# Optimization experiments

Hardware: AMD Instinct MI355X
Metric: run time of the kernel (lower is better)

## Reference

```python
import jax, jax.numpy as jnp
import numpy as np

B, C, N, H, K = 4, 128, 2048, 4, 20
_BN = np.float32(np.sqrt(1.0 + 1e-5))  # eval BatchNorm: running_mean=0, running_var=1


def setup_inputs() -> dict:
    key = jax.random.key(0)
    ks = jax.random.split(key, 16)
    r = lambda k, s: jax.random.normal(k, s, jnp.float32) * 0.1
    u = lambda k, s: jax.random.uniform(k, s, jnp.float32, 0.5, 1.5)
    return {
        "x": jax.random.normal(ks[0], (B, C, N, 1), jnp.float32),
        "fW": r(ks[1], (3, C, C)),
        "fb": r(ks[2], (3, C)),
        "fg": u(ks[3], (3, C)),
        "fbe": r(ks[4], (3, C)),
        "gW1": r(ks[5], (3, C, 2 * C)),
        "gb1": r(ks[6], (3, C)),
        "gg1": u(ks[7], (3, C)),
        "gbe1": r(ks[8], (3, C)),
        "gW2": r(ks[9], (3, C, C)),
        "gb2": r(ks[10], (3, C)),
        "gg2": u(ks[11], (3, C)),
        "gbe2": r(ks[12], (3, C)),
        "pW": r(ks[13], (C, C)),
        "pb": r(ks[14], (C,)),
        "temp": jnp.ones((H, 1, 1), jnp.float32),
        "num_heads": H,
        "k_num": K,
    }


def _filter(x, W, b, g, be):
    # x: [B,C,N]; 1x1 conv -> InstanceNorm(eps=1e-3) -> eval BatchNorm -> ReLU
    y = jnp.einsum('oc,bcn->bon', W, x) + b[:, None]
    m = jnp.mean(y, -1, keepdims=True)
    v = jnp.var(y, -1, keepdims=True)
    y = (y - m) / jnp.sqrt(v + 1e-3)
    return jax.nn.relu(y / _BN * g[:, None] + be[:, None])


def _knn(x, k):
    # x: [B,C,N]; topk of negative squared distance (self included)
    xx = jnp.sum(x * x, axis=1)                     # [B,N]
    inner = jnp.einsum('bcn,bcm->bnm', x, x)        # [B,N,N]
    pd = 2.0 * inner - xx[:, :, None] - xx[:, None, :]
    return jax.lax.top_k(pd, k)[1]                  # [B,N,k]


def _gcn(x, k, W1, b1, g1, be1, W2, b2, g2, be2):
    idx = _knn(x, k)
    xT = jnp.transpose(x, (0, 2, 1))                # [B,N,C]
    nb = jax.vmap(lambda p, i: p[i])(xT, idx)       # [B,N,k,C]
    ctr = jnp.broadcast_to(xT[:, :, None, :], nb.shape)
    feat = jnp.concatenate([ctr, ctr - nb], axis=-1)  # [B,N,k,2C]
    h = jnp.einsum('oi,bnki->bnko', W1, feat) + b1
    h = jax.nn.relu(h / _BN * g1 + be1)
    h = jnp.einsum('oi,bnki->bnko', W2, h) + b2
    h = jax.nn.relu(h / _BN * g2 + be2)
    return jnp.transpose(jnp.max(h, axis=2), (0, 2, 1))  # [B,C,N]


def _l2norm(x):
    n = jnp.sqrt(jnp.sum(x * x, axis=-1, keepdims=True))
    return x / jnp.maximum(n, 1e-12)


def reference(x, fW, fb, fg, fbe, gW1, gb1, gg1, gbe1, gW2, gb2, gg2, gbe2, pW, pb, temp, num_heads, k_num):
    xin = x[..., 0]                                 # [B,C,N]
    Bn, Cc, Nn = xin.shape
    qkv = []
    for i in range(3):  # q, k, v branches (structurally distinct params)
        f = _filter(xin, fW[i], fb[i], fg[i], fbe[i])
        g = _gcn(f, k_num, gW1[i], gb1[i], gg1[i], gbe1[i], gW2[i], gb2[i], gg2[i], gbe2[i])
        qkv.append(g.reshape(Bn, num_heads, Cc // num_heads, Nn))
    q, kk, v = qkv
    q = _l2norm(q)
    kk = _l2norm(kk)
    attn = jnp.einsum('bhcn,bhdn->bhcd', q, kk) * temp  # channel attention [B,H,c,c]
    attn = jax.nn.softmax(attn, axis=-1)
    out = jnp.einsum('bhcd,bhdn->bhcn', attn, v).reshape(Bn, Cc, Nn)
    out = jnp.einsum('oc,bcn->bon', pW, out) + pb[:, None]
    return (out + xin)[..., None]                   # [B,C,N,1]
```

## Files before the change

kernel.cpp:

```cpp
#include <hip/hip_runtime.h>
#include <math.h>


#define B_ 4
#define C_ 128
#define N_ 2048
#define H_ 4
#define K_ 20

typedef __bf16 bf16x8 __attribute__((ext_vector_type(8)));
typedef float f32x4 __attribute__((ext_vector_type(4)));
typedef unsigned int u32x4 __attribute__((ext_vector_type(4)));

__device__ __forceinline__ unsigned short f2bf(float f) {
    unsigned int u = __builtin_bit_cast(unsigned int, f);
    u += 0x7fffu + ((u >> 16) & 1u);
    return (unsigned short)(u >> 16);
}
__device__ __forceinline__ float bf2f(unsigned short s) {
    return __builtin_bit_cast(float, (unsigned int)s << 16);
}

#define PD_STRIDE 4194304
#define OFF_Y     0
#define OFF_P     0
#define OFF_Q     3145728
#define OFF_GT    6291456
#define OFF_AV    9437184
#define OFF_FT    16777216
#define OFF_SC    19922944
#define OFF_SH    19924480
#define OFF_XX    19926016
#define OFF_IDX   19950592
#define OFF_G     20442112
#define OFF_NRM   23587840
#define OFF_ATT   23588864

__global__ __launch_bounds__(256) void k_filter_conv(
    const float* __restrict__ x, const float* __restrict__ fW,
    const float* __restrict__ fb, float* __restrict__ y)
{
    __shared__ float Ws[8][C_];
    const int n = blockIdx.x * 256 + threadIdx.x;
    const int o0 = blockIdx.y * 8;
    const int iz = blockIdx.z;
    const int i = iz >> 2, b = iz & 3;
    for (int t = threadIdx.x; t < 8 * C_; t += 256) {
        const int j = t >> 7, c = t & 127;
        Ws[j][c] = fW[((size_t)i * C_ + o0 + j) * C_ + c];
    }
    __syncthreads();
    float acc[8] = {};
    const float* xb = x + ((size_t)b * C_) * N_ + n;
    #pragma unroll 4
    for (int c = 0; c < C_; ++c) {
        const float xv = xb[(size_t)c * N_];
        #pragma unroll
        for (int j = 0; j < 8; ++j) acc[j] += Ws[j][c] * xv;
    }
    float* yb = y + ((size_t)iz * C_ + o0) * N_ + n;
    #pragma unroll
    for (int j = 0; j < 8; ++j) yb[(size_t)j * N_] = acc[j] + fb[i * C_ + o0 + j];
}

__global__ __launch_bounds__(256) void k_rowstats(
    const float* __restrict__ y, const float* __restrict__ fg,
    const float* __restrict__ fbe, float* __restrict__ scale, float* __restrict__ shift)
{
    const int r = blockIdx.x;
    const int i = r >> 9, o = r & 127;
    const float* row = y + (size_t)r * N_;
    float s = 0.f, ss = 0.f;
    for (int n = threadIdx.x; n < N_; n += 256) {
        const float v = row[n];
        s += v; ss += v * v;
    }
    #pragma unroll
    for (int off = 32; off > 0; off >>= 1) {
        s += __shfl_down(s, off);
        ss += __shfl_down(ss, off);
    }
    __shared__ float red[2][4];
    const int wid = threadIdx.x >> 6;
    if ((threadIdx.x & 63) == 0) { red[0][wid] = s; red[1][wid] = ss; }
    __syncthreads();
    if (threadIdx.x == 0) {
        s = red[0][0] + red[0][1] + red[0][2] + red[0][3];
        ss = red[1][0] + red[1][1] + red[1][2] + red[1][3];
        const float mean = s * (1.f / N_);
        const float var = ss * (1.f / N_) - mean * mean;
        const float bn = sqrtf(1.00001f);
        const float sc = fg[i * C_ + o] / (bn * sqrtf(var + 1e-3f));
        scale[r] = sc;
        shift[r] = fbe[i * C_ + o] - mean * sc;
    }
}

__global__ __launch_bounds__(256) void k_norm_transpose(
    const float* __restrict__ y, const float* __restrict__ scale,
    const float* __restrict__ shift, float* __restrict__ fT,
    unsigned short* __restrict__ fH, unsigned short* __restrict__ fL)
{
    __shared__ float tile[32][33];
    const int n0 = blockIdx.x * 32, o0 = blockIdx.y * 32;
    const int iz = blockIdx.z;
    const int tx = threadIdx.x, ty = threadIdx.y;
    #pragma unroll
    for (int q = 0; q < 4; ++q) {
        const int o = o0 + ty + q * 8;
        const int r = iz * C_ + o;
        const float v = y[(size_t)r * N_ + n0 + tx] * scale[r] + shift[r];
        tile[ty + q * 8][tx] = fmaxf(v, 0.f);
    }
    __syncthreads();
    #pragma unroll
    for (int q = 0; q < 4; ++q) {
        const int n = n0 + ty + q * 8;
        const size_t idx = ((size_t)iz * N_ + n) * C_ + o0 + tx;
        const float v = tile[tx][ty + q * 8];
        fT[idx] = v;
        const unsigned short hi = f2bf(v);
        fH[idx] = hi;
        fL[idx] = f2bf(v - bf2f(hi));
    }
}

__global__ __launch_bounds__(256) void k_xx(const float* __restrict__ fT, float* __restrict__ xx)
{
    const int r = blockIdx.x * 256 + threadIdx.x;
    const float4* row = (const float4*)(fT + (size_t)r * C_);
    float s = 0.f;
    #pragma unroll
    for (int q = 0; q < C_ / 4; ++q) {
        const float4 v = row[q];
        s += v.x * v.x + v.y * v.y + v.z * v.z + v.w * v.w;
    }
    xx[r] = s;
}

__global__ __launch_bounds__(256) void k_pd_mfma(
    const unsigned short* __restrict__ fH, const unsigned short* __restrict__ fL,
    const float* __restrict__ xx, float* __restrict__ pdarena, int ib0)
{
    __shared__ __align__(16) unsigned short Ah[64 * C_], Al[64 * C_];
    __shared__ __align__(16) unsigned short Bh[64 * C_], Bl[64 * C_];
    const int j = blockIdx.z, ib = ib0 + j;
    const unsigned short* fHb = fH + (size_t)ib * N_ * C_;
    const unsigned short* fLb = fL + (size_t)ib * N_ * C_;
    const float* xxb = xx + ib * N_;
    float* pd = pdarena + (size_t)j * PD_STRIDE;
    const int n0 = blockIdx.x * 64, m0 = blockIdx.y * 64;
    const int t = threadIdx.x;
    {
        const int s = t & 15, rb = t >> 4;
        #pragma unroll
        for (int q = 0; q < 4; ++q) {
            const int r = rb + q * 16;
            const int ld = r * 256 + ((s * 16) ^ ((r & 7) << 4));
            *(u32x4*)((char*)Ah + ld) = *(const u32x4*)((const char*)fHb + (size_t)(n0 + r) * 256 + s * 16);
            *(u32x4*)((char*)Al + ld) = *(const u32x4*)((const char*)fLb + (size_t)(n0 + r) * 256 + s * 16);
            *(u32x4*)((char*)Bh + ld) = *(const u32x4*)((const char*)fHb + (size_t)(m0 + r) * 256 + s * 16);
            *(u32x4*)((char*)Bl + ld) = *(const u32x4*)((const char*)fLb + (size_t)(m0 + r) * 256 + s * 16);
        }
    }
    __syncthreads();
    const int lane = t & 63, w = t >> 6;
    const int lr = lane & 15, lg = lane >> 4;
    f32x4 acc[4];
    #pragma unroll
    for (int ct = 0; ct < 4; ++ct) acc[ct] = (f32x4){0.f, 0.f, 0.f, 0.f};
    #pragma unroll
    for (int ks = 0; ks < 4; ++ks) {
        const int arow = w * 16 + lr;
        const int cb = ks * 64 + lg * 16;
        const bf16x8 ah = __builtin_bit_cast(bf16x8,
            *(const u32x4*)((const char*)Ah + arow * 256 + (cb ^ ((arow & 7) << 4))));
        const bf16x8 al = __builtin_bit_cast(bf16x8,
            *(const u32x4*)((const char*)Al + arow * 256 + (cb ^ ((arow & 7) << 4))));
        #pragma unroll
        for (int ct = 0; ct < 4; ++ct) {
            const int brow = ct * 16 + lr;
            const int boff = brow * 256 + (cb ^ ((brow & 7) << 4));
            const bf16x8 bh = __builtin_bit_cast(bf16x8, *(const u32x4*)((const char*)Bh + boff));
            const bf16x8 bl = __builtin_bit_cast(bf16x8, *(const u32x4*)((const char*)Bl + boff));
            acc[ct] = __builtin_amdgcn_mfma_f32_16x16x32_bf16(ah, bh, acc[ct], 0, 0, 0);
            acc[ct] = __builtin_amdgcn_mfma_f32_16x16x32_bf16(ah, bl, acc[ct], 0, 0, 0);
            acc[ct] = __builtin_amdgcn_mfma_f32_16x16x32_bf16(al, bh, acc[ct], 0, 0, 0);
        }
    }
    #pragma unroll
    for (int ct = 0; ct < 4; ++ct) {
        const int m = m0 + ct * 16 + lr;
        const float xm = xxb[m];
        #pragma unroll
        for (int r = 0; r < 4; ++r) {
            const int n = n0 + w * 16 + lg * 4 + r;
            pd[(size_t)n * N_ + m] = 2.f * acc[ct][r] - xxb[n] - xm;
        }
    }
}

__global__ __launch_bounds__(256) void k_topk(
    const float* __restrict__ pdarena, int* __restrict__ idxb, int ib0)
{
    const int j = blockIdx.y;
    const float* pd = pdarena + (size_t)j * PD_STRIDE;
    const int lane = threadIdx.x & 63;
    const int n = blockIdx.x * 4 + (threadIdx.x >> 6);
    int* out = idxb + ((size_t)(ib0 + j) * N_ + n) * K_;
    const float* row = pd + (size_t)n * N_;
    float v[32];
    #pragma unroll
    for (int jj = 0; jj < 32; ++jj) v[jj] = row[jj * 64 + lane];
    for (int it = 0; it < K_; ++it) {
        float best = -3e38f; int bj = 0;
        #pragma unroll
        for (int jj = 0; jj < 32; ++jj) if (v[jj] > best) { best = v[jj]; bj = jj; }
        int bm = bj * 64 + lane;
        #pragma unroll
        for (int off = 1; off < 64; off <<= 1) {
            const float ov = __shfl_xor(best, off);
            const int   om = __shfl_xor(bm, off);
            if (ov > best || (ov == best && om < bm)) { best = ov; bm = om; }
        }
        if (lane == 0) out[it] = bm;
        if ((bm & 63) == lane) {
            const int jc = bm >> 6;
            #pragma unroll
            for (int jj = 0; jj < 32; ++jj) if (jj == jc) v[jj] = -3e38f;
        }
    }
}

__global__ __launch_bounds__(256) void k_pq(
    const float* __restrict__ fT, const float* __restrict__ gW1,
    float* __restrict__ P, float* __restrict__ Q)
{
    __shared__ float As[64][68], Bs[64][68];
    const int iz = blockIdx.z;
    const int i = iz >> 2;
    const int n0 = blockIdx.x * 64;
    const int yt = blockIdx.y;
    const bool isQ = (yt >= 2);
    const int oc0 = (yt & 1) * 64;
    const float* fTb = fT + (size_t)iz * N_ * C_;
    const int tm = threadIdx.x & 15, tn = threadIdx.x >> 4;
    float acc[4][4] = {};
    for (int kc = 0; kc < C_; kc += 64) {
        __syncthreads();
        #pragma unroll
        for (int q = 0; q < 4; ++q) {
            const int id = threadIdx.x + 256 * q;
            const int m = id >> 4, c4 = id & 15;
            const float4 va = *(const float4*)(fTb + ((size_t)(n0 + m)) * C_ + kc + c4 * 4);
            As[c4*4+0][m] = va.x; As[c4*4+1][m] = va.y; As[c4*4+2][m] = va.z; As[c4*4+3][m] = va.w;
            const float* wrow = gW1 + ((size_t)i * C_ + oc0 + m) * (2 * C_);
            const float4 wa = *(const float4*)(wrow + kc + c4 * 4);
            const float4 wb = *(const float4*)(wrow + C_ + kc + c4 * 4);
            float4 bv;
            if (isQ) { bv.x = -wb.x; bv.y = -wb.y; bv.z = -wb.z; bv.w = -wb.w; }
            else     { bv.x = wa.x + wb.x; bv.y = wa.y + wb.y; bv.z = wa.z + wb.z; bv.w = wa.w + wb.w; }
            Bs[c4*4+0][m] = bv.x; Bs[c4*4+1][m] = bv.y; Bs[c4*4+2][m] = bv.z; Bs[c4*4+3][m] = bv.w;
        }
        __syncthreads();
        #pragma unroll
        for (int k = 0; k < 64; ++k) {
            const float4 a  = *(const float4*)&As[k][tm * 4];
            const float4 bb = *(const float4*)&Bs[k][tn * 4];
            acc[0][0] += a.x*bb.x; acc[0][1] += a.x*bb.y; acc[0][2] += a.x*bb.z; acc[0][3] += a.x*bb.w;
            acc[1][0] += a.y*bb.x; acc[1][1] += a.y*bb.y; acc[1][2] += a.y*bb.z; acc[1][3] += a.y*bb.w;
            acc[2][0] += a.z*bb.x; acc[2][1] += a.z*bb.y; acc[2][2] += a.z*bb.z; acc[2][3] += a.z*bb.w;
            acc[3][0] += a.w*bb.x; acc[3][1] += a.w*bb.y; acc[3][2] += a.w*bb.z; acc[3][3] += a.w*bb.w;
        }
    }
    float* out = (isQ ? Q : P) + (size_t)iz * N_ * C_;
    #pragma unroll
    for (int rr = 0; rr < 4; ++rr) {
        const float4 st = make_float4(acc[rr][0], acc[rr][1], acc[rr][2], acc[rr][3]);
        *(float4*)(out + ((size_t)(n0 + tm * 4 + rr)) * C_ + oc0 + tn * 4) = st;
    }
}

__global__ __launch_bounds__(256) void k_edge2(
    const float* __restrict__ P, const float* __restrict__ Q, const int* __restrict__ idxb,
    const float* __restrict__ gb1, const float* __restrict__ gg1, const float* __restrict__ gbe1,
    const float* __restrict__ gW2, const float* __restrict__ gb2, const float* __restrict__ gg2,
    const float* __restrict__ gbe2, float* __restrict__ gT)
{
    __shared__ __align__(16) unsigned short h1s[160 * C_];
    __shared__ __align__(16) unsigned short W2s[C_ * C_];
    __shared__ float s1s[C_], t1s[C_], s2s[C_], t2s[C_];
    __shared__ int idxs[160];
    const int i = blockIdx.z, b = blockIdx.y;
    const int p0 = blockIdx.x * 8;
    const int t = threadIdx.x;
    const size_t base = (size_t)(i * B_ + b) * N_;

    if (t < C_) {
        const float bn = sqrtf(1.00001f);
        const float g1 = gg1[i * C_ + t];
        s1s[t] = g1 / bn;
        t1s[t] = gb1[i * C_ + t] * (g1 / bn) + gbe1[i * C_ + t];
        const float g2 = gg2[i * C_ + t];
        s2s[t] = g2 / bn;
        t2s[t] = gb2[i * C_ + t] * (g2 / bn) + gbe2[i * C_ + t];
    }
    if (t < 160) idxs[t] = idxb[base * K_ + p0 * K_ + t];
    __syncthreads();

    const int seg = t & 7;
    const int rb = t >> 3;
    float4 s1v[4], t1v[4];
    #pragma unroll
    for (int q = 0; q < 4; ++q) {
        s1v[q] = *(const float4*)&s1s[seg * 16 + q * 4];
        t1v[q] = *(const float4*)&t1s[seg * 16 + q * 4];
    }
    const float* Pb = P + base * C_;
    const float* Qb = Q + base * C_;
    #pragma unroll
    for (int it = 0; it < 5; ++it) {
        const int row = rb + 32 * it;
        const int p = row / 20;
        const int m = idxs[row];
        const float* Pr = Pb + (size_t)(p0 + p) * C_ + seg * 16;
        const float* Qr = Qb + (size_t)m * C_ + seg * 16;
        unsigned int pk[8];
        #pragma unroll
        for (int q = 0; q < 4; ++q) {
            const float4 pv = *(const float4*)(Pr + q * 4);
            const float4 qv = *(const float4*)(Qr + q * 4);
            const float r0 = fmaxf((pv.x + qv.x) * s1v[q].x + t1v[q].x, 0.f);
            const float r1 = fmaxf((pv.y + qv.y) * s1v[q].y + t1v[q].y, 0.f);
            const float r2 = fmaxf((pv.z + qv.z) * s1v[q].z + t1v[q].z, 0.f);
            const float r3 = fmaxf((pv.w + qv.w) * s1v[q].w + t1v[q].w, 0.f);
            pk[q * 2 + 0] = (unsigned int)f2bf(r0) | ((unsigned int)f2bf(r1) << 16);
            pk[q * 2 + 1] = (unsigned int)f2bf(r2) | ((unsigned int)f2bf(r3) << 16);
        }
        const int sw = (row & 7) << 4;
        char* bp = (char*)h1s + row * 256;
        *(u32x4*)(bp + ((seg * 32) ^ sw))      = (u32x4){pk[0], pk[1], pk[2], pk[3]};
        *(u32x4*)(bp + ((seg * 32 + 16) ^ sw)) = (u32x4){pk[4], pk[5], pk[6], pk[7]};
    }
    #pragma unroll
    for (int it = 0; it < 4; ++it) {
        const int o = rb + 32 * it;
        const float* wr = gW2 + ((size_t)i * C_ + o) * C_ + seg * 16;
        unsigned int pk[8];
        #pragma unroll
        for (int q = 0; q < 4; ++q) {
            const float4 wv = *(const float4*)(wr + q * 4);
            pk[q * 2 + 0] = (unsigned int)f2bf(wv.x) | ((unsigned int)f2bf(wv.y) << 16);
            pk[q * 2 + 1] = (unsigned int)f2bf(wv.z) | ((unsigned int)f2bf(wv.w) << 16);
        }
        const int sw = (o & 7) << 4;
        char* bp = (char*)W2s + o * 256;
        *(u32x4*)(bp + ((seg * 32) ^ sw))      = (u32x4){pk[0], pk[1], pk[2], pk[3]};
        *(u32x4*)(bp + ((seg * 32 + 16) ^ sw)) = (u32x4){pk[4], pk[5], pk[6], pk[7]};
    }
    __syncthreads();

    const int lane = t & 63, w = t >> 6;
    const int lr = lane & 15, lg = lane >> 4;
    bf16x8 Bf[2][4];
    #pragma unroll
    for (int nb = 0; nb < 2; ++nb)
        #pragma unroll
        for (int ks = 0; ks < 4; ++ks) {
            const int o = w * 32 + nb * 16 + lr;
            const int cb = ks * 64 + lg * 16;
            Bf[nb][ks] = __builtin_bit_cast(bf16x8,
                *(const u32x4*)((const char*)W2s + o * 256 + (cb ^ ((o & 7) << 4))));
        }
    f32x4 acc[10][2];
    #pragma unroll
    for (int mt = 0; mt < 10; ++mt)
        #pragma unroll
        for (int nb = 0; nb < 2; ++nb)
            acc[mt][nb] = (f32x4){0.f, 0.f, 0.f, 0.f};
    #pragma unroll
    for (int mt = 0; mt < 10; ++mt) {
        bf16x8 Af[4];
        #pragma unroll
        for (int ks = 0; ks < 4; ++ks) {
            const int row = mt * 16 + lr;
            const int cb = ks * 64 + lg * 16;
            Af[ks] = __builtin_bit_cast(bf16x8,
                *(const u32x4*)((const char*)h1s + row * 256 + (cb ^ ((row & 7) << 4))));
        }
        #pragma unroll
        for (int nb = 0; nb < 2; ++nb)
            #pragma unroll
            for (int ks = 0; ks < 4; ++ks)
                acc[mt][nb] = __builtin_amdgcn_mfma_f32_16x16x32_bf16(
                    Af[ks], Bf[nb][ks], acc[mt][nb], 0, 0, 0);
    }
    __syncthreads();

    #pragma unroll
    for (int mt = 0; mt < 10; ++mt)
        #pragma unroll
        for (int nb = 0; nb < 2; ++nb) {
            const int col = w * 32 + nb * 16 + lr;
            const float s2c = s2s[col], t2c = t2s[col];
            #pragma unroll
            for (int r = 0; r < 4; ++r) {
                const int row = mt * 16 + lg * 4 + r;
                const float v = fmaxf(acc[mt][nb][r] * s2c + t2c, 0.f);
                *(unsigned short*)((char*)h1s + row * 256 + ((col * 2) ^ ((row & 7) << 4))) = f2bf(v);
            }
        }
    __syncthreads();

    const int oc = t & 127, ph = t >> 7;
    float* gp = gT + (base + p0) * C_;
    #pragma unroll
    for (int pp = 0; pp < 4; ++pp) {
        const int p = ph * 4 + pp;
        float mx = 0.f;
        #pragma unroll
        for (int j = 0; j < 20; ++j) {
            const int row = p * 20 + j;
            const unsigned short us =
                *(const unsigned short*)((const char*)h1s + row * 256 + ((oc * 2) ^ ((row & 7) << 4)));
            mx = fmaxf(mx, bf2f(us));
        }
        gp[(size_t)p * C_ + oc] = mx;
    }
}

__global__ __launch_bounds__(256) void k_transpose2(
    const float* __restrict__ gT, float* __restrict__ g)
{
    __shared__ float tile[32][33];
    const int n0 = blockIdx.x * 32, o0 = blockIdx.y * 32;
    const int iz = blockIdx.z;
    const int tx = threadIdx.x, ty = threadIdx.y;
    #pragma unroll
    for (int q = 0; q < 4; ++q) {
        const int n = n0 + ty + q * 8;
        tile[ty + q * 8][tx] = gT[((size_t)iz * N_ + n) * C_ + o0 + tx];
    }
    __syncthreads();
    #pragma unroll
    for (int q = 0; q < 4; ++q) {
        const int o = o0 + ty + q * 8;
        g[((size_t)iz * C_ + o) * N_ + n0 + tx] = tile[tx][ty + q * 8];
    }
}

__global__ __launch_bounds__(256) void k_l2norm(const float* __restrict__ g, float* __restrict__ norms)
{
    const int r = blockIdx.x;
    const float* row = g + (size_t)r * N_;
    float s = 0.f;
    for (int n = threadIdx.x; n < N_; n += 256) { const float v = row[n]; s += v * v; }
    #pragma unroll
    for (int off = 32; off > 0; off >>= 1) s += __shfl_down(s, off);
    __shared__ float red[4];
    if ((threadIdx.x & 63) == 0) red[threadIdx.x >> 6] = s;
    __syncthreads();
    if (threadIdx.x == 0)
        norms[r] = fmaxf(sqrtf(red[0] + red[1] + red[2] + red[3]), 1e-12f);
}

__global__ __launch_bounds__(256) void k_attn(
    const float* __restrict__ g, const float* __restrict__ norms,
    const float* __restrict__ temp, float* __restrict__ attn)
{
    __shared__ float qs[N_];
    __shared__ float rowv[32];
    const int r = blockIdx.x;
    const int c = r & 31, h = (r >> 5) & 3, b = r >> 7;
    const float* qrow  = g + ((size_t)(0 * B_ + b) * C_ + h * 32 + c) * N_;
    const float* krows = g + ((size_t)(1 * B_ + b) * C_ + h * 32) * N_;
    for (int n = threadIdx.x; n < N_; n += 256) qs[n] = qrow[n];
    __syncthreads();
    const int d = threadIdx.x >> 3, s = threadIdx.x & 7;
    const float* kr = krows + (size_t)d * N_;
    float acc = 0.f;
    for (int m = 0; m < N_ / 32; ++m) {
        const int n = (m * 8 + s) * 4;
        const float4 kv = *(const float4*)(kr + n);
        acc += qs[n] * kv.x + qs[n+1] * kv.y + qs[n+2] * kv.z + qs[n+3] * kv.w;
    }
    #pragma unroll
    for (int off = 1; off < 8; off <<= 1) acc += __shfl_xor(acc, off);
    if (s == 0) rowv[d] = acc;
    __syncthreads();
    if (threadIdx.x < 32) {
        const int dd = threadIdx.x;
        const float nq = norms[(size_t)(0 * B_ + b) * C_ + h * 32 + c];
        const float nk = norms[(size_t)(1 * B_ + b) * C_ + h * 32 + dd];
        const float v = rowv[dd] / (nq * nk) * temp[h];
        float mx = v;
        #pragma unroll
        for (int off = 1; off < 32; off <<= 1) mx = fmaxf(mx, __shfl_xor(mx, off));
        const float e = expf(v - mx);
        float sm = e;
        #pragma unroll
        for (int off = 1; off < 32; off <<= 1) sm += __shfl_xor(sm, off);
        attn[(size_t)r * 32 + dd] = e / sm;
    }
}

__global__ __launch_bounds__(256) void k_av(
    const float* __restrict__ attn, const float* __restrict__ g, float* __restrict__ av)
{
    __shared__ float at[32][32];
    const int n = blockIdx.x * 256 + threadIdx.x;
    const int h = blockIdx.y, b = blockIdx.z;
    for (int t2 = threadIdx.x; t2 < 1024; t2 += 256)
        at[t2 >> 5][t2 & 31] = attn[((size_t)(b * H_ + h)) * 1024 + t2];
    __syncthreads();
    const float* vrows = g + ((size_t)(2 * B_ + b) * C_ + h * 32) * N_;
    float acc[32] = {};
    for (int dd = 0; dd < 32; ++dd) {
        const float vv = vrows[(size_t)dd * N_ + n];
        #pragma unroll
        for (int cc = 0; cc < 32; ++cc) acc[cc] += at[cc][dd] * vv;
    }
    float* avb = av + ((size_t)b * C_ + h * 32) * N_ + n;
    #pragma unroll
    for (int cc = 0; cc < 32; ++cc) avb[(size_t)cc * N_] = acc[cc];
}

__global__ __launch_bounds__(256) void k_proj(
    const float* __restrict__ av, const float* __restrict__ pW, const float* __restrict__ pb,
    const float* __restrict__ x, float* __restrict__ out)
{
    __shared__ float Ws[8][C_];
    const int n = blockIdx.x * 256 + threadIdx.x;
    const int o0 = blockIdx.y * 8;
    const int b = blockIdx.z;
    for (int t = threadIdx.x; t < 8 * C_; t += 256) {
        const int j = t >> 7, c = t & 127;
        Ws[j][c] = pW[(size_t)(o0 + j) * C_ + c];
    }
    __syncthreads();
    float acc[8] = {};
    const float* ab = av + ((size_t)b * C_) * N_ + n;
    #pragma unroll 4
    for (int c = 0; c < C_; ++c) {
        const float vv = ab[(size_t)c * N_];
        #pragma unroll
        for (int j = 0; j < 8; ++j) acc[j] += Ws[j][c] * vv;
    }
    #pragma unroll
    for (int j = 0; j < 8; ++j) {
        const int o = o0 + j;
        const size_t off = ((size_t)b * C_ + o) * N_ + n;
        out[off] = acc[j] + pb[o] + x[off];
    }
}

extern "C" void kernel_launch(void* const* d_in, const int* in_sizes, int n_in,
                              void* d_out, int out_size, void* d_ws, size_t ws_size,
                              hipStream_t stream)
{
    const float* x    = (const float*)d_in[0];
    const float* fW   = (const float*)d_in[1];
    const float* fb   = (const float*)d_in[2];
    const float* fg   = (const float*)d_in[3];
    const float* fbe  = (const float*)d_in[4];
    const float* gW1  = (const float*)d_in[5];
    const float* gb1  = (const float*)d_in[6];
    const float* gg1  = (const float*)d_in[7];
    const float* gbe1 = (const float*)d_in[8];
    const float* gW2  = (const float*)d_in[9];
    const float* gb2  = (const float*)d_in[10];
    const float* gg2  = (const float*)d_in[11];
    const float* gbe2 = (const float*)d_in[12];
    const float* pW   = (const float*)d_in[13];
    const float* pb   = (const float*)d_in[14];
    const float* temp = (const float*)d_in[15];
    float* ws = (float*)d_ws;

    float* arena = ws;
    float* y    = ws + OFF_Y;
    float* P    = ws + OFF_P;
    float* Q    = ws + OFF_Q;
    float* gT   = ws + OFF_GT;
    float* av   = ws + OFF_AV;
    float* fT   = ws + OFF_FT;
    float* sc   = ws + OFF_SC;
    float* sh   = ws + OFF_SH;
    float* xx   = ws + OFF_XX;
    int*   idxb = (int*)(ws + OFF_IDX);
    float* g    = ws + OFF_G;
    float* nrm  = ws + OFF_NRM;
    float* attn = ws + OFF_ATT;
    unsigned short* fH = (unsigned short*)g;
    unsigned short* fL = fH + (size_t)12 * N_ * C_;

    k_filter_conv<<<dim3(N_/256, C_/8, 12), 256, 0, stream>>>(x, fW, fb, y);
    k_rowstats<<<12 * C_, 256, 0, stream>>>(y, fg, fbe, sc, sh);
    k_norm_transpose<<<dim3(N_/32, C_/32, 12), dim3(32, 8), 0, stream>>>(y, sc, sh, fT, fH, fL);
    k_xx<<<(12 * N_) / 256, 256, 0, stream>>>(fT, xx);
    for (int g4 = 0; g4 < 3; ++g4) {
        k_pd_mfma<<<dim3(N_/64, N_/64, 4), 256, 0, stream>>>(fH, fL, xx, arena, g4 * 4);
        k_topk<<<dim3(N_/4, 4), 256, 0, stream>>>(arena, idxb, g4 * 4);
    }
    k_pq<<<dim3(N_/64, 4, 12), 256, 0, stream>>>(fT, gW1, P, Q);
    k_edge2<<<dim3(N_/8, B_, 3), 256, 0, stream>>>(P, Q, idxb, gb1, gg1, gbe1,
                                                   gW2, gb2, gg2, gbe2, gT);
    k_transpose2<<<dim3(N_/32, C_/32, 12), dim3(32, 8), 0, stream>>>(gT, g);
    k_l2norm<<<2 * B_ * C_, 256, 0, stream>>>(g, nrm);
    k_attn<<<B_ * H_ * 32, 256, 0, stream>>>(g, nrm, temp, attn);
    k_av<<<dim3(N_/256, H_, B_), 256, 0, stream>>>(attn, g, av);
    k_proj<<<dim3(N_/256, C_/8, B_), 256, 0, stream>>>(av, pW, pb, x, (float*)d_out);
    (void)in_sizes; (void)n_in; (void)out_size; (void)ws_size;
}
```

Measured before the change: 521.5 us.

## Move P/Q projection onto split-bf16 MFMA and drop fp32 transposed features

Replaces the scalar fp32 P/Q GEMM with a split-bf16 (hi/lo, three-product) MFMA kernel that reads the existing bf16 hi/lo feature buffers. Removes the fp32 transposed feature buffer and its writes, recomputing squared norms from hi+lo instead. Also widens the LDS XOR swizzle from 8 to 16 rows across all MFMA kernels to reduce bank conflicts. Accuracy of the P/Q and norm terms now depends on the hi/lo bf16 approximation, which drops the lo*lo term.

```diff
diff --git a/kernel.cpp b/kernel.cpp
--- a/kernel.cpp
+++ b/kernel.cpp
@@ -27,7 +27,6 @@
 #define OFF_Q     3145728
 #define OFF_GT    6291456
 #define OFF_AV    9437184
-#define OFF_FT    16777216
 #define OFF_SC    19922944
 #define OFF_SH    19924480
 #define OFF_XX    19926016
@@ -98,7 +97,7 @@
 
 __global__ __launch_bounds__(256) void k_norm_transpose(
     const float* __restrict__ y, const float* __restrict__ scale,
-    const float* __restrict__ shift, float* __restrict__ fT,
+    const float* __restrict__ shift,
     unsigned short* __restrict__ fH, unsigned short* __restrict__ fL)
 {
     __shared__ float tile[32][33];
@@ -118,22 +117,30 @@
         const int n = n0 + ty + q * 8;
         const size_t idx = ((size_t)iz * N_ + n) * C_ + o0 + tx;
         const float v = tile[tx][ty + q * 8];
-        fT[idx] = v;
         const unsigned short hi = f2bf(v);
         fH[idx] = hi;
         fL[idx] = f2bf(v - bf2f(hi));
     }
 }
 
-__global__ __launch_bounds__(256) void k_xx(const float* __restrict__ fT, float* __restrict__ xx)
+__global__ __launch_bounds__(256) void k_xx(
+    const unsigned short* __restrict__ fH, const unsigned short* __restrict__ fL,
+    float* __restrict__ xx)
 {
     const int r = blockIdx.x * 256 + threadIdx.x;
-    const float4* row = (const float4*)(fT + (size_t)r * C_);
+    const u32x4* rh = (const u32x4*)(fH + (size_t)r * C_);
+    const u32x4* rl = (const u32x4*)(fL + (size_t)r * C_);
     float s = 0.f;
     #pragma unroll
-    for (int q = 0; q < C_ / 4; ++q) {
-        const float4 v = row[q];
-        s += v.x * v.x + v.y * v.y + v.z * v.z + v.w * v.w;
+    for (int q = 0; q < 16; ++q) {
+        const u32x4 hv = rh[q], lv = rl[q];
+        #pragma unroll
+        for (int e = 0; e < 4; ++e) {
+            const unsigned int h = hv[e], l = lv[e];
+            const float v0 = bf2f((unsigned short)(h & 0xFFFFu)) + bf2f((unsigned short)(l & 0xFFFFu));
+            const float v1 = bf2f((unsigned short)(h >> 16)) + bf2f((unsigned short)(l >> 16));
+            s += v0 * v0 + v1 * v1;
+        }
     }
     xx[r] = s;
 }
@@ -156,7 +163,7 @@
         #pragma unroll
         for (int q = 0; q < 4; ++q) {
             const int r = rb + q * 16;
-            const int ld = r * 256 + ((s * 16) ^ ((r & 7) << 4));
+            const int ld = r * 256 + ((s * 16) ^ ((r & 15) << 4));
             *(u32x4*)((char*)Ah + ld) = *(const u32x4*)((const char*)fHb + (size_t)(n0 + r) * 256 + s * 16);
             *(u32x4*)((char*)Al + ld) = *(const u32x4*)((const char*)fLb + (size_t)(n0 + r) * 256 + s * 16);
             *(u32x4*)((char*)Bh + ld) = *(const u32x4*)((const char*)fHb + (size_t)(m0 + r) * 256 + s * 16);
@@ -174,13 +181,13 @@
         const int arow = w * 16 + lr;
         const int cb = ks * 64 + lg * 16;
         const bf16x8 ah = __builtin_bit_cast(bf16x8,
-            *(const u32x4*)((const char*)Ah + arow * 256 + (cb ^ ((arow & 7) << 4))));
+            *(const u32x4*)((const char*)Ah + arow * 256 + (cb ^ ((arow & 15) << 4))));
         const bf16x8 al = __builtin_bit_cast(bf16x8,
-            *(const u32x4*)((const char*)Al + arow * 256 + (cb ^ ((arow & 7) << 4))));
+            *(const u32x4*)((const char*)Al + arow * 256 + (cb ^ ((arow & 15) << 4))));
         #pragma unroll
         for (int ct = 0; ct < 4; ++ct) {
             const int brow = ct * 16 + lr;
-            const int boff = brow * 256 + (cb ^ ((brow & 7) << 4));
+            const int boff = brow * 256 + (cb ^ ((brow & 15) << 4));
             const bf16x8 bh = __builtin_bit_cast(bf16x8, *(const u32x4*)((const char*)Bh + boff));
             const bf16x8 bl = __builtin_bit_cast(bf16x8, *(const u32x4*)((const char*)Bl + boff));
             acc[ct] = __builtin_amdgcn_mfma_f32_16x16x32_bf16(ah, bh, acc[ct], 0, 0, 0);
@@ -232,52 +239,96 @@
     }
 }
 
-__global__ __launch_bounds__(256) void k_pq(
-    const float* __restrict__ fT, const float* __restrict__ gW1,
-    float* __restrict__ P, float* __restrict__ Q)
-{
-    __shared__ float As[64][68], Bs[64][68];
-    const int iz = blockIdx.z;
-    const int i = iz >> 2;
+__global__ __launch_bounds__(256) void k_pq_mfma(
+    const unsigned short* __restrict__ fH, const unsigned short* __restrict__ fL,
+    const float* __restrict__ gW1, float* __restrict__ P, float* __restrict__ Q)
+{
+    __shared__ __align__(16) unsigned short Ah[64 * C_], Al[64 * C_];
+    __shared__ __align__(16) unsigned short Bh[64 * C_], Bl[64 * C_];
+    const int iz = blockIdx.z, i = iz >> 2;
     const int n0 = blockIdx.x * 64;
     const int yt = blockIdx.y;
     const bool isQ = (yt >= 2);
     const int oc0 = (yt & 1) * 64;
-    const float* fTb = fT + (size_t)iz * N_ * C_;
-    const int tm = threadIdx.x & 15, tn = threadIdx.x >> 4;
-    float acc[4][4] = {};
-    for (int kc = 0; kc < C_; kc += 64) {
-        __syncthreads();
+    const int t = threadIdx.x;
+    const unsigned short* fHb = fH + (size_t)iz * N_ * C_;
+    const unsigned short* fLb = fL + (size_t)iz * N_ * C_;
+    {
+        const int s = t & 15, rb = t >> 4;
         #pragma unroll
         for (int q = 0; q < 4; ++q) {
-            const int id = threadIdx.x + 256 * q;
-            const int m = id >> 4, c4 = id & 15;
-            const float4 va = *(const float4*)(fTb + ((size_t)(n0 + m)) * C_ + kc + c4 * 4);
-            As[c4*4+0][m] = va.x; As[c4*4+1][m] = va.y; As[c4*4+2][m] = va.z; As[c4*4+3][m] = va.w;
-            const float* wrow = gW1 + ((size_t)i * C_ + oc0 + m) * (2 * C_);
-            const float4 wa = *(const float4*)(wrow + kc + c4 * 4);
-            const float4 wb = *(const float4*)(wrow + C_ + kc + c4 * 4);
-            float4 bv;
-            if (isQ) { bv.x = -wb.x; bv.y = -wb.y; bv.z = -wb.z; bv.w = -wb.w; }
-            else     { bv.x = wa.x + wb.x; bv.y = wa.y + wb.y; bv.z = wa.z + wb.z; bv.w = wa.w + wb.w; }
-            Bs[c4*4+0][m] = bv.x; Bs[c4*4+1][m] = bv.y; Bs[c4*4+2][m] = bv.z; Bs[c4*4+3][m] = bv.w;
-        }
-        __syncthreads();
-        #pragma unroll
-        for (int k = 0; k < 64; ++k) {
-            const float4 a  = *(const float4*)&As[k][tm * 4];
-            const float4 bb = *(const float4*)&Bs[k][tn * 4];
-            acc[0][0] += a.x*bb.x; acc[0][1] += a.x*bb.y; acc[0][2] += a.x*bb.z; acc[0][3] += a.x*bb.w;
-            acc[1][0] += a.y*bb.x; acc[1][1] += a.y*bb.y; acc[1][2] += a.y*bb.z; acc[1][3] += a.y*bb.w;
-            acc[2][0] += a.z*bb.x; acc[2][1] += a.z*bb.y; acc[2][2] += a.z*bb.z; acc[2][3] += a.z*bb.w;
-            acc[3][0] += a.w*bb.x; acc[3][1] += a.w*bb.y; acc[3][2] += a.w*bb.z; acc[3][3] += a.w*bb.w;
-        }
-    }
-    float* out = (isQ ? Q : P) + (size_t)iz * N_ * C_;
-    #pragma unroll
-    for (int rr = 0; rr < 4; ++rr) {
-        const float4 st = make_float4(acc[rr][0], acc[rr][1], acc[rr][2], acc[rr][3]);
-        *(float4*)(out + ((size_t)(n0 + tm * 4 + rr)) * C_ + oc0 + tn * 4) = st;
+            const int r = rb + q * 16;
+            const int ld = r * 256 + ((s * 16) ^ ((r & 15) << 4));
+            *(u32x4*)((char*)Ah + ld) = *(const u32x4*)((const char*)fHb + (size_t)(n0 + r) * 256 + s * 16);
+            *(u32x4*)((char*)Al + ld) = *(const u32x4*)((const char*)fLb + (size_t)(n0 + r) * 256 + s * 16);
+        }
+    }
+    {
+        const int cs = t & 15, ro = t >> 4;
+        #pragma unroll
+        for (int q = 0; q < 4; ++q) {
+            const int o = ro + q * 16;
+            const float* wrow = gW1 + ((size_t)i * C_ + oc0 + o) * (2 * C_) + cs * 8;
+            const float4 a0 = *(const float4*)(wrow);
+            const float4 a1 = *(const float4*)(wrow + 4);
+            const float4 b0 = *(const float4*)(wrow + C_);
+            const float4 b1 = *(const float4*)(wrow + C_ + 4);
+            float cmb[8];
+            if (isQ) {
+                cmb[0] = -b0.x; cmb[1] = -b0.y; cmb[2] = -b0.z; cmb[3] = -b0.w;
+                cmb[4] = -b1.x; cmb[5] = -b1.y; cmb[6] = -b1.z; cmb[7] = -b1.w;
+            } else {
+                cmb[0] = a0.x + b0.x; cmb[1] = a0.y + b0.y; cmb[2] = a0.z + b0.z; cmb[3] = a0.w + b0.w;
+                cmb[4] = a1.x + b1.x; cmb[5] = a1.y + b1.y; cmb[6] = a1.z + b1.z; cmb[7] = a1.w + b1.w;
+            }
+            unsigned int ph[4], pl[4];
+            #pragma unroll
+            for (int e = 0; e < 4; ++e) {
+                const unsigned short h0 = f2bf(cmb[e * 2 + 0]);
+                const unsigned short h1 = f2bf(cmb[e * 2 + 1]);
+                const unsigned short l0 = f2bf(cmb[e * 2 + 0] - bf2f(h0));
+                const unsigned short l1 = f2bf(cmb[e * 2 + 1] - bf2f(h1));
+                ph[e] = (unsigned int)h0 | ((unsigned int)h1 << 16);
+                pl[e] = (unsigned int)l0 | ((unsigned int)l1 << 16);
+            }
+            const int ld = o * 256 + ((cs * 16) ^ ((o & 15) << 4));
+            *(u32x4*)((char*)Bh + ld) = (u32x4){ph[0], ph[1], ph[2], ph[3]};
+            *(u32x4*)((char*)Bl + ld) = (u32x4){pl[0], pl[1], pl[2], pl[3]};
+        }
+    }
+    __syncthreads();
+    const int lane = t & 63, w = t >> 6;
+    const int lr = lane & 15, lg = lane >> 4;
+    f32x4 acc[4];
+    #pragma unroll
+    for (int ct = 0; ct < 4; ++ct) acc[ct] = (f32x4){0.f, 0.f, 0.f, 0.f};
+    #pragma unroll
+    for (int ks = 0; ks < 4; ++ks) {
+        const int arow = w * 16 + lr;
+        const int cb = ks * 64 + lg * 16;
+        const bf16x8 ah = __builtin_bit_cast(bf16x8,
+            *(const u32x4*)((const char*)Ah + arow * 256 + (cb ^ ((arow & 15) << 4))));
+        const bf16x8 al = __builtin_bit_cast(bf16x8,
+            *(const u32x4*)((const char*)Al + arow * 256 + (cb ^ ((arow & 15) << 4))));
+        #pragma unroll
+        for (int ct = 0; ct < 4; ++ct) {
+            const int brow = ct * 16 + lr;
+            const int boff = brow * 256 + (cb ^ ((brow & 15) << 4));
+            const bf16x8 bh = __builtin_bit_cast(bf16x8, *(const u32x4*)((const char*)Bh + boff));
+            const bf16x8 bl = __builtin_bit_cast(bf16x8, *(const u32x4*)((const char*)Bl + boff));
+            acc[ct] = __builtin_amdgcn_mfma_f32_16x16x32_bf16(ah, bh, acc[ct], 0, 0, 0);
+            acc[ct] = __builtin_amdgcn_mfma_f32_16x16x32_bf16(ah, bl, acc[ct], 0, 0, 0);
+            acc[ct] = __builtin_amdgcn_mfma_f32_16x16x32_bf16(al, bh, acc[ct], 0, 0, 0);
+        }
+    }
+    float* outp = (isQ ? Q : P) + (size_t)iz * N_ * C_;
+    #pragma unroll
+    for (int ct = 0; ct < 4; ++ct) {
+        #pragma unroll
+        for (int r = 0; r < 4; ++r) {
+            const int n = n0 + w * 16 + lg * 4 + r;
+            outp[(size_t)n * C_ + oc0 + ct * 16 + lr] = acc[ct][r];
+        }
     }
 }
 
@@ -337,7 +388,7 @@
             pk[q * 2 + 0] = (unsigned int)f2bf(r0) | ((unsigned int)f2bf(r1) << 16);
             pk[q * 2 + 1] = (unsigned int)f2bf(r2) | ((unsigned int)f2bf(r3) << 16);
         }
-        const int sw = (row & 7) << 4;
+        const int sw = (row & 15) << 4;
         char* bp = (char*)h1s + row * 256;
         *(u32x4*)(bp + ((seg * 32) ^ sw))      = (u32x4){pk[0], pk[1], pk[2], pk[3]};
         *(u32x4*)(bp + ((seg * 32 + 16) ^ sw)) = (u32x4){pk[4], pk[5], pk[6], pk[7]};
@@ -353,7 +404,7 @@
             pk[q * 2 + 0] = (unsigned int)f2bf(wv.x) | ((unsigned int)f2bf(wv.y) << 16);
             pk[q * 2 + 1] = (unsigned int)f2bf(wv.z) | ((unsigned int)f2bf(wv.w) << 16);
         }
-        const int sw = (o & 7) << 4;
+        const int sw = (o & 15) << 4;
         char* bp = (char*)W2s + o * 256;
         *(u32x4*)(bp + ((seg * 32) ^ sw))      = (u32x4){pk[0], pk[1], pk[2], pk[3]};
         *(u32x4*)(bp + ((seg * 32 + 16) ^ sw)) = (u32x4){pk[4], pk[5], pk[6], pk[7]};
@@ -370,7 +421,7 @@
             const int o = w * 32 + nb * 16 + lr;
             const int cb = ks * 64 + lg * 16;
             Bf[nb][ks] = __builtin_bit_cast(bf16x8,
-                *(const u32x4*)((const char*)W2s + o * 256 + (cb ^ ((o & 7) << 4))));
+                *(const u32x4*)((const char*)W2s + o * 256 + (cb ^ ((o & 15) << 4))));
         }
     f32x4 acc[10][2];
     #pragma unroll
@@ -386,7 +437,7 @@
             const int row = mt * 16 + lr;
             const int cb = ks * 64 + lg * 16;
             Af[ks] = __builtin_bit_cast(bf16x8,
-                *(const u32x4*)((const char*)h1s + row * 256 + (cb ^ ((row & 7) << 4))));
+                *(const u32x4*)((const char*)h1s + row * 256 + (cb ^ ((row & 15) << 4))));
         }
         #pragma unroll
         for (int nb = 0; nb < 2; ++nb)
@@ -407,7 +458,7 @@
             for (int r = 0; r < 4; ++r) {
                 const int row = mt * 16 + lg * 4 + r;
                 const float v = fmaxf(acc[mt][nb][r] * s2c + t2c, 0.f);
-                *(unsigned short*)((char*)h1s + row * 256 + ((col * 2) ^ ((row & 7) << 4))) = f2bf(v);
+                *(unsigned short*)((char*)h1s + row * 256 + ((col * 2) ^ ((row & 15) << 4))) = f2bf(v);
             }
         }
     __syncthreads();
@@ -422,7 +473,7 @@
         for (int j = 0; j < 20; ++j) {
             const int row = p * 20 + j;
             const unsigned short us =
-                *(const unsigned short*)((const char*)h1s + row * 256 + ((oc * 2) ^ ((row & 7) << 4)));
+                *(const unsigned short*)((const char*)h1s + row * 256 + ((oc * 2) ^ ((row & 15) << 4)));
             mx = fmaxf(mx, bf2f(us));
         }
         gp[(size_t)p * C_ + oc] = mx;
@@ -582,7 +633,6 @@
     float* Q    = ws + OFF_Q;
     float* gT   = ws + OFF_GT;
     float* av   = ws + OFF_AV;
-    float* fT   = ws + OFF_FT;
     float* sc   = ws + OFF_SC;
     float* sh   = ws + OFF_SH;
     float* xx   = ws + OFF_XX;
@@ -595,13 +645,13 @@
 
     k_filter_conv<<<dim3(N_/256, C_/8, 12), 256, 0, stream>>>(x, fW, fb, y);
     k_rowstats<<<12 * C_, 256, 0, stream>>>(y, fg, fbe, sc, sh);
-    k_norm_transpose<<<dim3(N_/32, C_/32, 12), dim3(32, 8), 0, stream>>>(y, sc, sh, fT, fH, fL);
-    k_xx<<<(12 * N_) / 256, 256, 0, stream>>>(fT, xx);
+    k_norm_transpose<<<dim3(N_/32, C_/32, 12), dim3(32, 8), 0, stream>>>(y, sc, sh, fH, fL);
+    k_xx<<<(12 * N_) / 256, 256, 0, stream>>>(fH, fL, xx);
     for (int g4 = 0; g4 < 3; ++g4) {
         k_pd_mfma<<<dim3(N_/64, N_/64, 4), 256, 0, stream>>>(fH, fL, xx, arena, g4 * 4);
         k_topk<<<dim3(N_/4, 4), 256, 0, stream>>>(arena, idxb, g4 * 4);
     }
-    k_pq<<<dim3(N_/64, 4, 12), 256, 0, stream>>>(fT, gW1, P, Q);
+    k_pq_mfma<<<dim3(N_/64, 4, 12), 256, 0, stream>>>(fH, fL, gW1, P, Q);
     k_edge2<<<dim3(N_/8, B_, 3), 256, 0, stream>>>(P, Q, idxb, gb1, gg1, gbe1,
                                                    gW2, gb2, gg2, gbe2, gT);
     k_transpose2<<<dim3(N_/32, C_/32, 12), dim3(32, 8), 0, stream>>>(gT, g);
```

Result: faster. 499.8 us (-4.2%).
